# Performance work log

Measured on AMD Instinct MI355X. Metric: run time of the kernel, lower is better.

Reference implementation:

```python
import jax, jax.numpy as jnp
import numpy as np

D_MODEL = 1024
NUM_HEADS = 16
HEAD_DIM = D_MODEL // NUM_HEADS
B, T_Q, T_KV = 4, 4096, 4096


def setup_inputs() -> dict:
    key = jax.random.key(0)
    ks = jax.random.split(key, 10)
    s_in = 1.0 / np.sqrt(D_MODEL)
    s_out = 1.0 / np.sqrt(D_MODEL)
    return {
        "q": jax.random.normal(ks[0], (B, T_Q, D_MODEL), jnp.float32),
        "kv": jax.random.normal(ks[1], (B, T_KV, D_MODEL), jnp.float32),
        # per-head projection weights stacked: [H, d_model, head_dim]
        "Wq": jax.random.uniform(ks[2], (NUM_HEADS, D_MODEL, HEAD_DIM), jnp.float32, -s_in, s_in),
        "bq": jax.random.uniform(ks[3], (NUM_HEADS, HEAD_DIM), jnp.float32, -s_in, s_in),
        "Wk": jax.random.uniform(ks[4], (NUM_HEADS, D_MODEL, HEAD_DIM), jnp.float32, -s_in, s_in),
        "bk": jax.random.uniform(ks[5], (NUM_HEADS, HEAD_DIM), jnp.float32, -s_in, s_in),
        "Wv": jax.random.uniform(ks[6], (NUM_HEADS, D_MODEL, HEAD_DIM), jnp.float32, -s_in, s_in),
        "bv": jax.random.uniform(ks[7], (NUM_HEADS, HEAD_DIM), jnp.float32, -s_in, s_in),
        "Wo": jax.random.uniform(ks[8], (D_MODEL, D_MODEL), jnp.float32, -s_out, s_out),
        "bo": jax.random.uniform(ks[9], (D_MODEL,), jnp.float32, -s_out, s_out),
    }


def reference(q, kv, Wq, bq, Wk, bk, Wv, bv, Wo, bo):
    Bsz, Tq, _ = q.shape
    # per-head projections fused into one batched GEMM each: [b,t,d] x [h,d,e] -> [b,h,t,e]
    qh = jnp.einsum('btd,hde->bhte', q, Wq) + bq[None, :, None, :]
    kh = jnp.einsum('btd,hde->bhte', kv, Wk) + bk[None, :, None, :]
    vh = jnp.einsum('btd,hde->bhte', kv, Wv) + bv[None, :, None, :]
    # squared feature map
    qh = qh * qh
    kh = kh * kh
    # O(N) linear attention aggregation
    kv_sum = jnp.einsum('bhnd,bhne->bhde', kh, vh)           # [B,H,e,e]
    z = 1.0 / (jnp.einsum('bhnd,bhd->bhn', qh, kh.sum(axis=2)) + 1e-6)  # [B,H,Tq]
    attn = jnp.einsum('bhnd,bhde,bhn->bhne', qh, kv_sum, z)  # [B,H,Tq,e]
    attn = attn.transpose(0, 2, 1, 3).reshape(Bsz, Tq, D_MODEL)
    return attn @ Wo.T + bo
```

## Files before the change

kernel.cpp:

```cpp
#include <hip/hip_runtime.h>

#define BSZ 4
#define TSEQ 4096
#define DM 1024
#define NH 16
#define HD 64
#define BT (BSZ * TSEQ)
#define INV_LOSCALE (1.0f / 4096.0f)

using f32x4 = __attribute__((ext_vector_type(4))) float;
using f16x8 = __attribute__((ext_vector_type(8))) _Float16;
using u32x2 = __attribute__((ext_vector_type(2))) unsigned;
using u32x4 = __attribute__((ext_vector_type(4))) unsigned;

typedef const __attribute__((address_space(1))) void* gas_ptr;
typedef __attribute__((address_space(3))) void* las_ptr;

__device__ __forceinline__ void gload16(const void* g, void* l) {
    __builtin_amdgcn_global_load_lds((gas_ptr)g, (las_ptr)l, 16, 0, 0);
}

__device__ __forceinline__ void split1(float x, _Float16& h, _Float16& l) {
    h = (_Float16)x;
    l = (_Float16)((x - (float)h) * 4096.0f);
}
__device__ __forceinline__ unsigned pack2(_Float16 a, _Float16 b) {
    return (unsigned)__builtin_bit_cast(unsigned short, a) |
           ((unsigned)__builtin_bit_cast(unsigned short, b) << 16);
}
__device__ __forceinline__ f32x4 mfma_f16(f16x8 a, f16x8 b, f32x4 c) {
    return __builtin_amdgcn_mfma_f32_16x16x32_f16(a, b, c, 0, 0, 0);
}

__global__ __launch_bounds__(256) void fragsplit_kernel(const float* __restrict__ in,
        _Float16* __restrict__ hi, _Float16* __restrict__ lo) {
    const int C = blockIdx.x * 256 + threadIdx.x;
    const int l15 = C & 15, quad = (C >> 4) & 3, rb = (C >> 6) & 3;
    const int s = (C >> 8) & 31, panel = C >> 13;
    const size_t src = ((size_t)(panel * 64 + rb * 16 + l15)) * DM + s * 32 + quad * 8;
    f32x4 v0 = *(const f32x4*)&in[src];
    f32x4 v1 = *(const f32x4*)&in[src + 4];
    _Float16 h[8], l[8];
    #pragma unroll
    for (int j = 0; j < 4; ++j) { split1(v0[j], h[j], l[j]); split1(v1[j], h[4 + j], l[4 + j]); }
    ((u32x4*)hi)[C] = (u32x4){pack2(h[0],h[1]), pack2(h[2],h[3]), pack2(h[4],h[5]), pack2(h[6],h[7])};
    ((u32x4*)lo)[C] = (u32x4){pack2(l[0],l[1]), pack2(l[2],l[3]), pack2(l[4],l[5]), pack2(l[6],l[7])};
}

__global__ __launch_bounds__(256) void wsplit_kernel(
    const float* __restrict__ Wq, const float* __restrict__ Wk, const float* __restrict__ Wv,
    _Float16* __restrict__ qh, _Float16* __restrict__ ql,
    _Float16* __restrict__ kh, _Float16* __restrict__ kl,
    _Float16* __restrict__ vh, _Float16* __restrict__ vl) {
    const int tid = threadIdx.x;
    const int k0 = blockIdx.x * 64, h = blockIdx.y, w = blockIdx.z;
    const float* __restrict__ W = (w == 0) ? Wq : (w == 1) ? Wk : Wv;
    _Float16* __restrict__ dh = (w == 0) ? qh : (w == 1) ? kh : vh;
    _Float16* __restrict__ dl = (w == 0) ? ql : (w == 1) ? kl : vl;
    __shared__ __align__(16) float ws_[64][68];
    #pragma unroll
    for (int it = 0; it < 4; ++it) {
        int idx = it * 256 + tid;
        int r = idx >> 4, c4 = (idx & 15) * 4;
        *(f32x4*)&ws_[r][c4] = *(const f32x4*)&W[((size_t)h * DM + k0 + r) * HD + c4];
    }
    __syncthreads();
    const int n = tid >> 2, kq16 = (tid & 3) * 16;
    _Float16 hh[16], ll[16];
    #pragma unroll
    for (int j = 0; j < 16; ++j) split1(ws_[kq16 + j][n], hh[j], ll[j]);
    #pragma unroll
    for (int c = 0; c < 2; ++c) {
        int kg = k0 + kq16 + c * 8;
        int s = kg >> 5, quad = (kg >> 3) & 3;
        size_t chunk = (size_t)(h * 32 + s) * 256 + ((n >> 4) * 4 + quad) * 16 + (n & 15);
        ((u32x4*)dh)[chunk] = (u32x4){pack2(hh[c*8+0],hh[c*8+1]), pack2(hh[c*8+2],hh[c*8+3]),
                                      pack2(hh[c*8+4],hh[c*8+5]), pack2(hh[c*8+6],hh[c*8+7])};
        ((u32x4*)dl)[chunk] = (u32x4){pack2(ll[c*8+0],ll[c*8+1]), pack2(ll[c*8+2],ll[c*8+3]),
                                      pack2(ll[c*8+4],ll[c*8+5]), pack2(ll[c*8+6],ll[c*8+7])};
    }
}

__global__ __launch_bounds__(256, 3) void kv_stats_kernel(
    const _Float16* __restrict__ kv_hi, const _Float16* __restrict__ kv_lo,
    const _Float16* __restrict__ wkt_hi, const _Float16* __restrict__ wkt_lo,
    const _Float16* __restrict__ wvt_hi, const _Float16* __restrict__ wvt_lo,
    const float* __restrict__ bk, const float* __restrict__ bv,
    float* __restrict__ kv_sum, float* __restrict__ ksum)
{
    const int tid = threadIdx.x;
    const int lane = tid & 63, wave = tid >> 6, quad = lane >> 4, l15 = lane & 15;
    const int b = blockIdx.z, h = blockIdx.y, bx = blockIdx.x;

    __shared__ __align__(16) char smem[49152];
    float* khs = (float*)smem;
    float* vhs = (float*)(smem + 16384);

    const int isV = wave >> 1, w1 = wave & 1;
    const size_t btile = (size_t)h * 32;
    const int ty = tid >> 4, tx = tid & 15;

    f32x4 akv[4] = {};
    float aks[4] = {0.f, 0.f, 0.f, 0.f};

    for (int sub = 0; sub < 4; ++sub) {
        const size_t atile = (size_t)(b * 64 + bx * 4 + sub) * 32;
        auto stage = [&](int p, int s) {
            char* dst = smem + p * 24576 + tid * 16;
            const size_t ao = (atile + s) * 2048 + tid * 8;
            const size_t bo = (btile + s) * 2048 + tid * 8;
            gload16(&kv_hi[ao],  dst);
            gload16(&kv_lo[ao],  dst + 4096);
            gload16(&wkt_hi[bo], dst + 8192);
            gload16(&wkt_lo[bo], dst + 12288);
            gload16(&wvt_hi[bo], dst + 16384);
            gload16(&wvt_lo[bo], dst + 20480);
        };

        f32x4 acc_h[2][4] = {}, acc_c[2][4] = {};
        stage(0, 0);
        for (int s = 0; s < 32; ++s) {
            const int p = s & 1;
            if (s < 31) {
                stage(p ^ 1, s + 1);
                asm volatile("s_waitcnt vmcnt(6)" ::: "memory");
            } else {
                asm volatile("s_waitcnt vmcnt(0)" ::: "memory");
            }
            __builtin_amdgcn_s_barrier();
            __builtin_amdgcn_sched_barrier(0);
            const char* bufc = smem + p * 24576;
            const _Float16* a_hi = (const _Float16*)bufc;
            const _Float16* a_lo = (const _Float16*)(bufc + 4096);
            const _Float16* bh = (const _Float16*)(bufc + (isV ? 16384 : 8192));
            const _Float16* bl = (const _Float16*)(bufc + (isV ? 20480 : 12288));
            f16x8 afh[2], afl[2], bfh[4], bfl[4];
            #pragma unroll
            for (int mt = 0; mt < 2; ++mt) {
                afh[mt] = *(const f16x8*)&a_hi[(w1 * 2 + mt) * 512 + lane * 8];
                afl[mt] = *(const f16x8*)&a_lo[(w1 * 2 + mt) * 512 + lane * 8];
            }
            #pragma unroll
            for (int nt = 0; nt < 4; ++nt) {
                bfh[nt] = *(const f16x8*)&bh[nt * 512 + lane * 8];
                bfl[nt] = *(const f16x8*)&bl[nt * 512 + lane * 8];
            }
            #pragma unroll
            for (int mt = 0; mt < 2; ++mt)
                #pragma unroll
                for (int nt = 0; nt < 4; ++nt) {
                    acc_h[mt][nt] = mfma_f16(afh[mt], bfh[nt], acc_h[mt][nt]);
                    acc_c[mt][nt] = mfma_f16(afh[mt], bfl[nt], acc_c[mt][nt]);
                    acc_c[mt][nt] = mfma_f16(afl[mt], bfh[nt], acc_c[mt][nt]);
                }
            __builtin_amdgcn_s_barrier();
            __builtin_amdgcn_sched_barrier(0);
        }

        {
            const float* __restrict__ bias = (isV ? bv : bk) + h * HD;
            float* __restrict__ outs = isV ? vhs : khs;
            float bia[4];
            #pragma unroll
            for (int nt = 0; nt < 4; ++nt) bia[nt] = bias[nt * 16 + l15];
            #pragma unroll
            for (int mt = 0; mt < 2; ++mt)
                #pragma unroll
                for (int nt = 0; nt < 4; ++nt)
                    #pragma unroll
                    for (int r = 0; r < 4; ++r) {
                        int t = w1 * 32 + mt * 16 + quad * 4 + r;
                        float v = acc_h[mt][nt][r] + INV_LOSCALE * acc_c[mt][nt][r] + bia[nt];
                        if (!isV) v = v * v;
                        outs[t * 64 + nt * 16 + l15] = v;
                    }
        }
        __syncthreads();

        #pragma unroll 4
        for (int t = 0; t < 64; ++t) {
            f32x4 kd = *(const f32x4*)&khs[t * 64 + ty * 4];
            f32x4 ve = *(const f32x4*)&vhs[t * 64 + tx * 4];
            #pragma unroll
            for (int i = 0; i < 4; ++i) {
                aks[i] += kd[i];
                akv[i] += kd[i] * ve;
            }
        }
        __syncthreads();
    }

    float* kvp = kv_sum + (size_t)(b * NH + h) * HD * HD;
    #pragma unroll
    for (int i = 0; i < 4; ++i)
        #pragma unroll
        for (int j = 0; j < 4; ++j)
            atomicAdd(&kvp[(ty * 4 + i) * HD + tx * 4 + j], akv[i][j]);
    if (tx == 0) {
        float* ksp = ksum + (b * NH + h) * HD;
        #pragma unroll
        for (int i = 0; i < 4; ++i) atomicAdd(&ksp[ty * 4 + i], aks[i]);
    }
}

__global__ __launch_bounds__(256, 3) void q_attn_ps_kernel(
    const _Float16* __restrict__ qf_hi, const _Float16* __restrict__ qf_lo,
    const _Float16* __restrict__ wqt_hi, const _Float16* __restrict__ wqt_lo,
    const float* __restrict__ bq,
    const float* __restrict__ kv_sum, const float* __restrict__ ksum,
    _Float16* __restrict__ attn_hi, _Float16* __restrict__ attn_lo)
{
    const int tid = threadIdx.x;
    const int lane = tid & 63, wave = tid >> 6, quad = lane >> 4, l15 = lane & 15;
    const int b = blockIdx.z, h = blockIdx.y, bx = blockIdx.x;

    __shared__ __align__(16) char smem[32768];
    __shared__ __align__(16) float qs[64 * 68];
    __shared__ float z_s[64], ks_s[64];

    if (tid < 64) ks_s[tid] = ksum[(b * NH + h) * HD + tid];

    const size_t atile = (size_t)(b * 64 + bx) * 32;
    const size_t btile = (size_t)h * 32;

    auto stage = [&](int p, int s) {
        char* dst = smem + p * 16384 + tid * 16;
        const size_t ao = (atile + s) * 2048 + tid * 8;
        const size_t bo = (btile + s) * 2048 + tid * 8;
        gload16(&qf_hi[ao],  dst);
        gload16(&qf_lo[ao],  dst + 4096);
        gload16(&wqt_hi[bo], dst + 8192);
        gload16(&wqt_lo[bo], dst + 12288);
    };

    f32x4 acc_h[4] = {}, acc_c[4] = {};
    stage(0, 0);
    for (int s = 0; s < 32; ++s) {
        const int p = s & 1;
        if (s < 31) {
            stage(p ^ 1, s + 1);
            asm volatile("s_waitcnt vmcnt(4)" ::: "memory");
        } else {
            asm volatile("s_waitcnt vmcnt(0)" ::: "memory");
        }
        __builtin_amdgcn_s_barrier();
        __builtin_amdgcn_sched_barrier(0);
        const char* bufc = smem + p * 16384;
        f16x8 afh = *(const f16x8*)((const _Float16*)bufc + wave * 512 + lane * 8);
        f16x8 afl = *(const f16x8*)((const _Float16*)(bufc + 4096) + wave * 512 + lane * 8);
        f16x8 bfh[4], bfl[4];
        #pragma unroll
        for (int nt = 0; nt < 4; ++nt) {
            bfh[nt] = *(const f16x8*)((const _Float16*)(bufc + 8192) + nt * 512 + lane * 8);
            bfl[nt] = *(const f16x8*)((const _Float16*)(bufc + 12288) + nt * 512 + lane * 8);
        }
        #pragma unroll
        for (int nt = 0; nt < 4; ++nt) {
            acc_h[nt] = mfma_f16(afh, bfh[nt], acc_h[nt]);
            acc_c[nt] = mfma_f16(afh, bfl[nt], acc_c[nt]);
            acc_c[nt] = mfma_f16(afl, bfh[nt], acc_c[nt]);
        }
        __builtin_amdgcn_s_barrier();
        __builtin_amdgcn_sched_barrier(0);
    }

    {
        const int mrow0 = wave * 16;
        const float* __restrict__ bias = bq + h * HD;
        float zp[4] = {0.f, 0.f, 0.f, 0.f};
        #pragma unroll
        for (int nt = 0; nt < 4; ++nt) {
            int d = nt * 16 + l15;
            float bia = bias[d];
            float ks  = ks_s[d];
            #pragma unroll
            for (int r = 0; r < 4; ++r) {
                int t = mrow0 + quad * 4 + r;
                float v = acc_h[nt][r] + INV_LOSCALE * acc_c[nt][r] + bia;
                float v2 = v * v;
                qs[t * 68 + d] = v2;
                zp[r] = fmaf(v2, ks, zp[r]);
            }
        }
        #pragma unroll
        for (int r = 0; r < 4; ++r) {
            float p = zp[r];
            p += __shfl_xor(p, 1);
            p += __shfl_xor(p, 2);
            p += __shfl_xor(p, 4);
            p += __shfl_xor(p, 8);
            if (l15 == 0) z_s[mrow0 + quad * 4 + r] = 1.f / (p + 1e-6f);
        }
    }
    __syncthreads();

    float* kvs = (float*)smem;
    {
        const float* __restrict__ kvp = kv_sum + (size_t)(b * NH + h) * HD * HD;
        #pragma unroll
        for (int it = 0; it < 4; ++it) {
            int idx = it * 256 + tid;
            int r = idx >> 4, c = (idx & 15) * 4;
            *(f32x4*)&kvs[r * 64 + c] = *(const f32x4*)&kvp[r * HD + c];
        }
    }
    __syncthreads();

    const int ty = tid >> 4, tx = tid & 15;
    f32x4 sv[4] = {};
    #pragma unroll 4
    for (int d = 0; d < 64; d += 4) {
        f32x4 b0 = *(const f32x4*)&kvs[(d + 0) * 64 + tx * 4];
        f32x4 b1 = *(const f32x4*)&kvs[(d + 1) * 64 + tx * 4];
        f32x4 b2 = *(const f32x4*)&kvs[(d + 2) * 64 + tx * 4];
        f32x4 b3 = *(const f32x4*)&kvs[(d + 3) * 64 + tx * 4];
        #pragma unroll
        for (int i = 0; i < 4; ++i) {
            f32x4 av = *(const f32x4*)&qs[(ty * 4 + i) * 68 + d];
            sv[i] += av.x * b0 + av.y * b1 + av.z * b2 + av.w * b3;
        }
    }
    const size_t opanel = (size_t)b * 64 + bx;
    const int s_out = h * 2 + (tx >> 3);
    const int kq = (tx >> 1) & 3;
    const int rem8 = (tx & 1) * 8;
    #pragma unroll
    for (int i = 0; i < 4; ++i) {
        int t = ty * 4 + i;
        f32x4 o = sv[i] * z_s[t];
        _Float16 hh[4], ll[4];
        #pragma unroll
        for (int j = 0; j < 4; ++j) split1(o[j], hh[j], ll[j]);
        size_t cb = (((opanel * 32 + s_out) * 256 + ((t >> 4) * 4 + kq) * 16 + (t & 15)) << 4) + rem8;
        *(u32x2*)((char*)attn_hi + cb) = (u32x2){pack2(hh[0], hh[1]), pack2(hh[2], hh[3])};
        *(u32x2*)((char*)attn_lo + cb) = (u32x2){pack2(ll[0], ll[1]), pack2(ll[2], ll[3])};
    }
}

__global__ __launch_bounds__(256, 3) void q_attn_kernel(
    const float* __restrict__ q,
    const _Float16* __restrict__ wqt_hi, const _Float16* __restrict__ wqt_lo,
    const float* __restrict__ bq,
    const float* __restrict__ kv_sum, const float* __restrict__ ksum,
    _Float16* __restrict__ attn_hi, _Float16* __restrict__ attn_lo)
{
    const int tid = threadIdx.x;
    const int lane = tid & 63, wave = tid >> 6, quad = lane >> 4, l15 = lane & 15;
    const int b = blockIdx.z, h = blockIdx.y, bx = blockIdx.x;
    const int t0 = bx * 64;

    __shared__ __align__(16) char smem[32768];
    __shared__ __align__(16) float qs[64 * 68];
    __shared__ float z_s[64], ks_s[64];

    if (tid < 64) ks_s[tid] = ksum[(b * NH + h) * HD + tid];

    const int arb = tid >> 6, aquad = (tid >> 4) & 3, al15 = tid & 15;
    const float* __restrict__ qrow =
        q + ((size_t)b * TSEQ + t0 + arb * 16 + al15) * DM + aquad * 8;
    const size_t btile = (size_t)h * 32;

    auto asplit_write = [&](int p, f32x4 v0, f32x4 v1) {
        _Float16 hh[8], ll[8];
        #pragma unroll
        for (int j = 0; j < 4; ++j) { split1(v0[j], hh[j], ll[j]); split1(v1[j], hh[4+j], ll[4+j]); }
        char* dst = smem + p * 16384 + tid * 16;
        *(u32x4*)dst =
            (u32x4){pack2(hh[0],hh[1]), pack2(hh[2],hh[3]), pack2(hh[4],hh[5]), pack2(hh[6],hh[7])};
        *(u32x4*)(dst + 4096) =
            (u32x4){pack2(ll[0],ll[1]), pack2(ll[2],ll[3]), pack2(ll[4],ll[5]), pack2(ll[6],ll[7])};
    };
    auto stageB = [&](int p, int s) {
        char* dst = smem + p * 16384 + 8192 + tid * 16;
        const size_t bo = (btile + s) * 2048 + tid * 8;
        gload16(&wqt_hi[bo], dst);
        gload16(&wqt_lo[bo], dst + 4096);
    };

    f32x4 acc_h[4] = {}, acc_c[4] = {};
    f32x4 v0 = *(const f32x4*)&qrow[0];
    f32x4 v1 = *(const f32x4*)&qrow[4];
    asplit_write(0, v0, v1);
    stageB(0, 0);
    v0 = *(const f32x4*)&qrow[32];
    v1 = *(const f32x4*)&qrow[36];
    asm volatile("s_waitcnt vmcnt(2) lgkmcnt(0)" ::: "memory");
    __builtin_amdgcn_s_barrier();
    __builtin_amdgcn_sched_barrier(0);

    for (int s = 0; s < 32; ++s) {
        const int p = s & 1;
        if (s < 31) {
            stageB(p ^ 1, s + 1);
            asplit_write(p ^ 1, v0, v1);
            if (s < 30) {
                v0 = *(const f32x4*)&qrow[(s + 2) * 32];
                v1 = *(const f32x4*)&qrow[(s + 2) * 32 + 4];
            }
            asm volatile("s_waitcnt vmcnt(4) lgkmcnt(0)" ::: "memory");
        } else {
            asm volatile("s_waitcnt vmcnt(0)" ::: "memory");
        }
        __builtin_amdgcn_s_barrier();
        __builtin_amdgcn_sched_barrier(0);
        const char* bufc = smem + p * 16384;
        f16x8 afh = *(const f16x8*)((const _Float16*)bufc + wave * 512 + lane * 8);
        f16x8 afl = *(const f16x8*)((const _Float16*)(bufc + 4096) + wave * 512 + lane * 8);
        f16x8 bfh[4], bfl[4];
        #pragma unroll
        for (int nt = 0; nt < 4; ++nt) {
            bfh[nt] = *(const f16x8*)((const _Float16*)(bufc + 8192) + nt * 512 + lane * 8);
            bfl[nt] = *(const f16x8*)((const _Float16*)(bufc + 12288) + nt * 512 + lane * 8);
        }
        #pragma unroll
        for (int nt = 0; nt < 4; ++nt) {
            acc_h[nt] = mfma_f16(afh, bfh[nt], acc_h[nt]);
            acc_c[nt] = mfma_f16(afh, bfl[nt], acc_c[nt]);
            acc_c[nt] = mfma_f16(afl, bfh[nt], acc_c[nt]);
        }
        __builtin_amdgcn_s_barrier();
        __builtin_amdgcn_sched_barrier(0);
    }

    {
        const int mrow0 = wave * 16;
        const float* __restrict__ bias = bq + h * HD;
        float zp[4] = {0.f, 0.f, 0.f, 0.f};
        #pragma unroll
        for (int nt = 0; nt < 4; ++nt) {
            int d = nt * 16 + l15;
            float bia = bias[d];
            float ks  = ks_s[d];
            #pragma unroll
            for (int r = 0; r < 4; ++r) {
                int t = mrow0 + quad * 4 + r;
                float v = acc_h[nt][r] + INV_LOSCALE * acc_c[nt][r] + bia;
                float v2 = v * v;
                qs[t * 68 + d] = v2;
                zp[r] = fmaf(v2, ks, zp[r]);
            }
        }
        #pragma unroll
        for (int r = 0; r < 4; ++r) {
            float p = zp[r];
            p += __shfl_xor(p, 1);
            p += __shfl_xor(p, 2);
            p += __shfl_xor(p, 4);
            p += __shfl_xor(p, 8);
            if (l15 == 0) z_s[mrow0 + quad * 4 + r] = 1.f / (p + 1e-6f);
        }
    }
    __syncthreads();

    float* kvs = (float*)smem;
    {
        const float* __restrict__ kvp = kv_sum + (size_t)(b * NH + h) * HD * HD;
        #pragma unroll
        for (int it = 0; it < 4; ++it) {
            int idx = it * 256 + tid;
            int r = idx >> 4, c = (idx & 15) * 4;
            *(f32x4*)&kvs[r * 64 + c] = *(const f32x4*)&kvp[r * HD + c];
        }
    }
    __syncthreads();

    const int ty = tid >> 4, tx = tid & 15;
    f32x4 sv[4] = {};
    #pragma unroll 4
    for (int d = 0; d < 64; d += 4) {
        f32x4 b0 = *(const f32x4*)&kvs[(d + 0) * 64 + tx * 4];
        f32x4 b1 = *(const f32x4*)&kvs[(d + 1) * 64 + tx * 4];
        f32x4 b2 = *(const f32x4*)&kvs[(d + 2) * 64 + tx * 4];
        f32x4 b3 = *(const f32x4*)&kvs[(d + 3) * 64 + tx * 4];
        #pragma unroll
        for (int i = 0; i < 4; ++i) {
            f32x4 av = *(const f32x4*)&qs[(ty * 4 + i) * 68 + d];
            sv[i] += av.x * b0 + av.y * b1 + av.z * b2 + av.w * b3;
        }
    }
    const size_t opanel = (size_t)b * 64 + bx;
    const int s_out = h * 2 + (tx >> 3);
    const int kq = (tx >> 1) & 3;
    const int rem8 = (tx & 1) * 8;
    #pragma unroll
    for (int i = 0; i < 4; ++i) {
        int t = ty * 4 + i;
        f32x4 o = sv[i] * z_s[t];
        _Float16 hh[4], ll[4];
        #pragma unroll
        for (int j = 0; j < 4; ++j) split1(o[j], hh[j], ll[j]);
        size_t cb = (((opanel * 32 + s_out) * 256 + ((t >> 4) * 4 + kq) * 16 + (t & 15)) << 4) + rem8;
        *(u32x2*)((char*)attn_hi + cb) = (u32x2){pack2(hh[0], hh[1]), pack2(hh[2], hh[3])};
        *(u32x2*)((char*)attn_lo + cb) = (u32x2){pack2(ll[0], ll[1]), pack2(ll[2], ll[3])};
    }
}

__global__ __launch_bounds__(256, 3) void out_proj_kernel(
    const _Float16* __restrict__ attn_hi, const _Float16* __restrict__ attn_lo,
    const _Float16* __restrict__ wo_hi, const _Float16* __restrict__ wo_lo,
    const float* __restrict__ bo, float* __restrict__ out)
{
    const int tid = threadIdx.x;
    const int lane = tid & 63, wave = tid >> 6, quad = lane >> 4, l15 = lane & 15;
    const int n0 = blockIdx.x * 64;
    const size_t m0 = (size_t)blockIdx.y * 128;

    __shared__ __align__(16) char smem[49152];
    float* cs = (float*)smem;

    const size_t ap0 = (m0 >> 6) * 32, ap1 = ap0 + 32;
    const size_t bpn = (size_t)(n0 >> 6) * 32;

    auto stage = [&](int p, int s) {
        char* dst = smem + p * 24576 + tid * 16;
        const size_t co = (size_t)s * 2048 + tid * 8;
        gload16(&attn_hi[ap0 * 2048 + co], dst);
        gload16(&attn_hi[ap1 * 2048 + co], dst + 4096);
        gload16(&attn_lo[ap0 * 2048 + co], dst + 8192);
        gload16(&attn_lo[ap1 * 2048 + co], dst + 12288);
        gload16(&wo_hi[bpn * 2048 + co],  dst + 16384);
        gload16(&wo_lo[bpn * 2048 + co],  dst + 20480);
    };

    const int panel = wave >> 1;
    f32x4 acc_h[2][4] = {}, acc_c[2][4] = {};
    stage(0, 0);
    for (int s = 0; s < 32; ++s) {
        const int p = s & 1;
        if (s < 31) {
            stage(p ^ 1, s + 1);
            asm volatile("s_waitcnt vmcnt(6)" ::: "memory");
        } else {
            asm volatile("s_waitcnt vmcnt(0)" ::: "memory");
        }
        __builtin_amdgcn_s_barrier();
        __builtin_amdgcn_sched_barrier(0);
        const char* bufc = smem + p * 24576;
        f16x8 afh[2], afl[2], bfh[4], bfl[4];
        #pragma unroll
        for (int mt = 0; mt < 2; ++mt) {
            int rbl = (wave & 1) * 2 + mt;
            afh[mt] = *(const f16x8*)((const _Float16*)(bufc + panel * 4096) + rbl * 512 + lane * 8);
            afl[mt] = *(const f16x8*)((const _Float16*)(bufc + 8192 + panel * 4096) + rbl * 512 + lane * 8);
        }
        #pragma unroll
        for (int nt = 0; nt < 4; ++nt) {
            bfh[nt] = *(const f16x8*)((const _Float16*)(bufc + 16384) + nt * 512 + lane * 8);
            bfl[nt] = *(const f16x8*)((const _Float16*)(bufc + 20480) + nt * 512 + lane * 8);
        }
        #pragma unroll
        for (int mt = 0; mt < 2; ++mt)
            #pragma unroll
            for (int nt = 0; nt < 4; ++nt) {
                acc_h[mt][nt] = mfma_f16(afh[mt], bfh[nt], acc_h[mt][nt]);
                acc_c[mt][nt] = mfma_f16(afh[mt], bfl[nt], acc_c[mt][nt]);
                acc_c[mt][nt] = mfma_f16(afl[mt], bfh[nt], acc_c[mt][nt]);
            }
        __builtin_amdgcn_s_barrier();
        __builtin_amdgcn_sched_barrier(0);
    }

    {
        float bia[4];
        #pragma unroll
        for (int nt = 0; nt < 4; ++nt) bia[nt] = bo[n0 + nt * 16 + l15];
        #pragma unroll
        for (int mt = 0; mt < 2; ++mt)
            #pragma unroll
            for (int nt = 0; nt < 4; ++nt)
                #pragma unroll
                for (int r = 0; r < 4; ++r) {
                    int t = wave * 32 + mt * 16 + quad * 4 + r;
                    cs[t * 64 + nt * 16 + l15] =
                        acc_h[mt][nt][r] + INV_LOSCALE * acc_c[mt][nt][r] + bia[nt];
                }
    }
    __syncthreads();
    #pragma unroll
    for (int it = 0; it < 8; ++it) {
        int idx = it * 256 + tid;
        int r = idx >> 4, c = (idx & 15) * 4;
        *(f32x4*)&out[(m0 + r) * DM + n0 + c] = *(f32x4*)&cs[r * 64 + c];
    }
}

extern "C" void kernel_launch(void* const* d_in, const int* in_sizes, int n_in,
                              void* d_out, int out_size, void* d_ws, size_t ws_size,
                              hipStream_t stream) {
    const float* q  = (const float*)d_in[0];
    const float* kv = (const float*)d_in[1];
    const float* Wq = (const float*)d_in[2];
    const float* bq = (const float*)d_in[3];
    const float* Wk = (const float*)d_in[4];
    const float* bk = (const float*)d_in[5];
    const float* Wv = (const float*)d_in[6];
    const float* bv = (const float*)d_in[7];
    const float* Wo = (const float*)d_in[8];
    const float* bo = (const float*)d_in[9];
    float* out = (float*)d_out;

    char* p = (char*)d_ws;
    float* kv_sum = (float*)p;              p += (size_t)BSZ * NH * HD * HD * 4;
    float* ksum   = (float*)p;              p += (size_t)BSZ * NH * HD * 4;
    _Float16* wqt_hi = (_Float16*)p;        p += (size_t)NH * HD * DM * 2;
    _Float16* wqt_lo = (_Float16*)p;        p += (size_t)NH * HD * DM * 2;
    _Float16* wkt_hi = (_Float16*)p;        p += (size_t)NH * HD * DM * 2;
    _Float16* wkt_lo = (_Float16*)p;        p += (size_t)NH * HD * DM * 2;
    _Float16* wvt_hi = (_Float16*)p;        p += (size_t)NH * HD * DM * 2;
    _Float16* wvt_lo = (_Float16*)p;        p += (size_t)NH * HD * DM * 2;
    _Float16* wo_hi  = (_Float16*)p;        p += (size_t)DM * DM * 2;
    _Float16* wo_lo  = (_Float16*)p;        p += (size_t)DM * DM * 2;
    _Float16* buf_hi = (_Float16*)p;        p += (size_t)BT * DM * 2;
    _Float16* buf_lo = (_Float16*)p;        p += (size_t)BT * DM * 2;
    _Float16* qf_hi  = (_Float16*)p;        p += (size_t)BT * DM * 2;
    _Float16* qf_lo  = (_Float16*)p;        p += (size_t)BT * DM * 2;
    const bool big = ws_size >= (size_t)(p - (char*)d_ws);

    size_t zero_bytes = ((size_t)BSZ * NH * HD * HD + (size_t)BSZ * NH * HD) * sizeof(float);
    hipMemsetAsync(d_ws, 0, zero_bytes, stream);

    fragsplit_kernel<<<(BT * DM / 8) / 256, 256, 0, stream>>>(kv, buf_hi, buf_lo);
    wsplit_kernel<<<dim3(DM / 64, NH, 3), 256, 0, stream>>>(
        Wq, Wk, Wv, wqt_hi, wqt_lo, wkt_hi, wkt_lo, wvt_hi, wvt_lo);
    fragsplit_kernel<<<(DM * DM / 8) / 256, 256, 0, stream>>>(Wo, wo_hi, wo_lo);
    if (big)
        fragsplit_kernel<<<(BT * DM / 8) / 256, 256, 0, stream>>>(q, qf_hi, qf_lo);

    kv_stats_kernel<<<dim3(TSEQ / 256, NH, BSZ), 256, 0, stream>>>(
        buf_hi, buf_lo, wkt_hi, wkt_lo, wvt_hi, wvt_lo, bk, bv, kv_sum, ksum);
    if (big)
        q_attn_ps_kernel<<<dim3(TSEQ / 64, NH, BSZ), 256, 0, stream>>>(
            qf_hi, qf_lo, wqt_hi, wqt_lo, bq, kv_sum, ksum, buf_hi, buf_lo);
    else
        q_attn_kernel<<<dim3(TSEQ / 64, NH, BSZ), 256, 0, stream>>>(
            q, wqt_hi, wqt_lo, bq, kv_sum, ksum, buf_hi, buf_lo);
    out_proj_kernel<<<dim3(DM / 64, BT / 128), 256, 0, stream>>>(
        buf_hi, buf_lo, wo_hi, wo_lo, bo, out);
}
```

Before: 735.7 us.

## Double row tiles in kv_stats and q_attn_ps kernels to reuse weight fragments

Both projection GEMM kernels now load two 64-row activation panels per stage, so each staged weight tile is used against twice as many rows. kv_stats processes 128 rows per sub-iteration with 4x4 accumulators per wave and lowers occupancy to 2 blocks; q_attn_ps handles 128 rows per block with half the grid. The aim is to cut redundant weight-tile loads and barrier overhead per row. The cost is higher register and LDS pressure, lower occupancy, and fewer blocks for the q kernel. The q fragsplit launch is also moved after kv_stats.

```diff
diff --git a/kernel.cpp b/kernel.cpp
--- a/kernel.cpp
+++ b/kernel.cpp
@@ -81,7 +81,7 @@
     }
 }
 
-__global__ __launch_bounds__(256, 3) void kv_stats_kernel(
+__global__ __launch_bounds__(256, 2) void kv_stats_kernel(
     const _Float16* __restrict__ kv_hi, const _Float16* __restrict__ kv_lo,
     const _Float16* __restrict__ wkt_hi, const _Float16* __restrict__ wkt_lo,
     const _Float16* __restrict__ wvt_hi, const _Float16* __restrict__ wvt_lo,
@@ -92,53 +92,56 @@
     const int lane = tid & 63, wave = tid >> 6, quad = lane >> 4, l15 = lane & 15;
     const int b = blockIdx.z, h = blockIdx.y, bx = blockIdx.x;
 
-    __shared__ __align__(16) char smem[49152];
+    __shared__ __align__(16) char smem[65536];
     float* khs = (float*)smem;
-    float* vhs = (float*)(smem + 16384);
-
-    const int isV = wave >> 1, w1 = wave & 1;
+    float* vhs = (float*)(smem + 32768);
+
+    const int isV = wave >> 1, half = wave & 1;
     const size_t btile = (size_t)h * 32;
     const int ty = tid >> 4, tx = tid & 15;
 
     f32x4 akv[4] = {};
     float aks[4] = {0.f, 0.f, 0.f, 0.f};
 
-    for (int sub = 0; sub < 4; ++sub) {
-        const size_t atile = (size_t)(b * 64 + bx * 4 + sub) * 32;
+    for (int sub = 0; sub < 2; ++sub) {
+        const size_t apan = (size_t)(b * 64 + bx * 4 + sub * 2);
         auto stage = [&](int p, int s) {
-            char* dst = smem + p * 24576 + tid * 16;
-            const size_t ao = (atile + s) * 2048 + tid * 8;
+            char* dst = smem + p * 32768 + tid * 16;
+            const size_t a0 = (apan * 32 + s) * 2048 + tid * 8;
+            const size_t a1 = ((apan + 1) * 32 + s) * 2048 + tid * 8;
             const size_t bo = (btile + s) * 2048 + tid * 8;
-            gload16(&kv_hi[ao],  dst);
-            gload16(&kv_lo[ao],  dst + 4096);
-            gload16(&wkt_hi[bo], dst + 8192);
-            gload16(&wkt_lo[bo], dst + 12288);
-            gload16(&wvt_hi[bo], dst + 16384);
-            gload16(&wvt_lo[bo], dst + 20480);
+            gload16(&kv_hi[a0], dst);
+            gload16(&kv_hi[a1], dst + 4096);
+            gload16(&kv_lo[a0], dst + 8192);
+            gload16(&kv_lo[a1], dst + 12288);
+            gload16(&wkt_hi[bo], dst + 16384);
+            gload16(&wkt_lo[bo], dst + 20480);
+            gload16(&wvt_hi[bo], dst + 24576);
+            gload16(&wvt_lo[bo], dst + 28672);
         };
 
-        f32x4 acc_h[2][4] = {}, acc_c[2][4] = {};
+        f32x4 acc_h[4][4] = {}, acc_c[4][4] = {};
         stage(0, 0);
         for (int s = 0; s < 32; ++s) {
             const int p = s & 1;
             if (s < 31) {
                 stage(p ^ 1, s + 1);
-                asm volatile("s_waitcnt vmcnt(6)" ::: "memory");
+                asm volatile("s_waitcnt vmcnt(8)" ::: "memory");
             } else {
                 asm volatile("s_waitcnt vmcnt(0)" ::: "memory");
             }
             __builtin_amdgcn_s_barrier();
             __builtin_amdgcn_sched_barrier(0);
-            const char* bufc = smem + p * 24576;
+            const char* bufc = smem + p * 32768;
             const _Float16* a_hi = (const _Float16*)bufc;
-            const _Float16* a_lo = (const _Float16*)(bufc + 4096);
-            const _Float16* bh = (const _Float16*)(bufc + (isV ? 16384 : 8192));
-            const _Float16* bl = (const _Float16*)(bufc + (isV ? 20480 : 12288));
-            f16x8 afh[2], afl[2], bfh[4], bfl[4];
-            #pragma unroll
-            for (int mt = 0; mt < 2; ++mt) {
-                afh[mt] = *(const f16x8*)&a_hi[(w1 * 2 + mt) * 512 + lane * 8];
-                afl[mt] = *(const f16x8*)&a_lo[(w1 * 2 + mt) * 512 + lane * 8];
+            const _Float16* a_lo = (const _Float16*)(bufc + 8192);
+            const _Float16* bh = (const _Float16*)(bufc + (isV ? 24576 : 16384));
+            const _Float16* bl = (const _Float16*)(bufc + (isV ? 28672 : 20480));
+            f16x8 afh[4], afl[4], bfh[4], bfl[4];
+            #pragma unroll
+            for (int mt = 0; mt < 4; ++mt) {
+                afh[mt] = *(const f16x8*)&a_hi[half * 2048 + mt * 512 + lane * 8];
+                afl[mt] = *(const f16x8*)&a_lo[half * 2048 + mt * 512 + lane * 8];
             }
             #pragma unroll
             for (int nt = 0; nt < 4; ++nt) {
@@ -146,7 +149,7 @@
                 bfl[nt] = *(const f16x8*)&bl[nt * 512 + lane * 8];
             }
             #pragma unroll
-            for (int mt = 0; mt < 2; ++mt)
+            for (int mt = 0; mt < 4; ++mt)
                 #pragma unroll
                 for (int nt = 0; nt < 4; ++nt) {
                     acc_h[mt][nt] = mfma_f16(afh[mt], bfh[nt], acc_h[mt][nt]);
@@ -164,12 +167,12 @@
             #pragma unroll
             for (int nt = 0; nt < 4; ++nt) bia[nt] = bias[nt * 16 + l15];
             #pragma unroll
-            for (int mt = 0; mt < 2; ++mt)
+            for (int mt = 0; mt < 4; ++mt)
                 #pragma unroll
                 for (int nt = 0; nt < 4; ++nt)
                     #pragma unroll
                     for (int r = 0; r < 4; ++r) {
-                        int t = w1 * 32 + mt * 16 + quad * 4 + r;
+                        int t = half * 64 + mt * 16 + quad * 4 + r;
                         float v = acc_h[mt][nt][r] + INV_LOSCALE * acc_c[mt][nt][r] + bia[nt];
                         if (!isV) v = v * v;
                         outs[t * 64 + nt * 16 + l15] = v;
@@ -178,7 +181,7 @@
         __syncthreads();
 
         #pragma unroll 4
-        for (int t = 0; t < 64; ++t) {
+        for (int t = 0; t < 128; ++t) {
             f32x4 kd = *(const f32x4*)&khs[t * 64 + ty * 4];
             f32x4 ve = *(const f32x4*)&vhs[t * 64 + tx * 4];
             #pragma unroll
@@ -214,87 +217,101 @@
     const int lane = tid & 63, wave = tid >> 6, quad = lane >> 4, l15 = lane & 15;
     const int b = blockIdx.z, h = blockIdx.y, bx = blockIdx.x;
 
-    __shared__ __align__(16) char smem[32768];
-    __shared__ __align__(16) float qs[64 * 68];
-    __shared__ float z_s[64], ks_s[64];
+    __shared__ __align__(16) char smem[51200];
+    __shared__ float z_s[128], ks_s[64];
 
     if (tid < 64) ks_s[tid] = ksum[(b * NH + h) * HD + tid];
 
-    const size_t atile = (size_t)(b * 64 + bx) * 32;
+    const size_t apan = (size_t)(b * 64 + bx * 2);
     const size_t btile = (size_t)h * 32;
 
     auto stage = [&](int p, int s) {
-        char* dst = smem + p * 16384 + tid * 16;
-        const size_t ao = (atile + s) * 2048 + tid * 8;
+        char* dst = smem + p * 24576 + tid * 16;
+        const size_t a0 = (apan * 32 + s) * 2048 + tid * 8;
+        const size_t a1 = ((apan + 1) * 32 + s) * 2048 + tid * 8;
         const size_t bo = (btile + s) * 2048 + tid * 8;
-        gload16(&qf_hi[ao],  dst);
-        gload16(&qf_lo[ao],  dst + 4096);
-        gload16(&wqt_hi[bo], dst + 8192);
-        gload16(&wqt_lo[bo], dst + 12288);
+        gload16(&qf_hi[a0], dst);
+        gload16(&qf_hi[a1], dst + 4096);
+        gload16(&qf_lo[a0], dst + 8192);
+        gload16(&qf_lo[a1], dst + 12288);
+        gload16(&wqt_hi[bo], dst + 16384);
+        gload16(&wqt_lo[bo], dst + 20480);
     };
 
-    f32x4 acc_h[4] = {}, acc_c[4] = {};
+    f32x4 acc_h[2][4] = {}, acc_c[2][4] = {};
     stage(0, 0);
     for (int s = 0; s < 32; ++s) {
         const int p = s & 1;
         if (s < 31) {
             stage(p ^ 1, s + 1);
-            asm volatile("s_waitcnt vmcnt(4)" ::: "memory");
+            asm volatile("s_waitcnt vmcnt(6)" ::: "memory");
         } else {
             asm volatile("s_waitcnt vmcnt(0)" ::: "memory");
         }
         __builtin_amdgcn_s_barrier();
         __builtin_amdgcn_sched_barrier(0);
-        const char* bufc = smem + p * 16384;
-        f16x8 afh = *(const f16x8*)((const _Float16*)bufc + wave * 512 + lane * 8);
-        f16x8 afl = *(const f16x8*)((const _Float16*)(bufc + 4096) + wave * 512 + lane * 8);
-        f16x8 bfh[4], bfl[4];
+        const char* bufc = smem + p * 24576;
+        const _Float16* a_hi = (const _Float16*)bufc;
+        const _Float16* a_lo = (const _Float16*)(bufc + 8192);
+        f16x8 afh[2], afl[2], bfh[4], bfl[4];
+        #pragma unroll
+        for (int mt = 0; mt < 2; ++mt) {
+            int fo = (wave * 2 + mt) * 512 + lane * 8;
+            afh[mt] = *(const f16x8*)&a_hi[fo];
+            afl[mt] = *(const f16x8*)&a_lo[fo];
+        }
         #pragma unroll
         for (int nt = 0; nt < 4; ++nt) {
-            bfh[nt] = *(const f16x8*)((const _Float16*)(bufc + 8192) + nt * 512 + lane * 8);
-            bfl[nt] = *(const f16x8*)((const _Float16*)(bufc + 12288) + nt * 512 + lane * 8);
-        }
-        #pragma unroll
-        for (int nt = 0; nt < 4; ++nt) {
-            acc_h[nt] = mfma_f16(afh, bfh[nt], acc_h[nt]);
-            acc_c[nt] = mfma_f16(afh, bfl[nt], acc_c[nt]);
-            acc_c[nt] = mfma_f16(afl, bfh[nt], acc_c[nt]);
-        }
+            bfh[nt] = *(const f16x8*)((const _Float16*)(bufc + 16384) + nt * 512 + lane * 8);
+            bfl[nt] = *(const f16x8*)((const _Float16*)(bufc + 20480) + nt * 512 + lane * 8);
+        }
+        #pragma unroll
+        for (int mt = 0; mt < 2; ++mt)
+            #pragma unroll
+            for (int nt = 0; nt < 4; ++nt) {
+                acc_h[mt][nt] = mfma_f16(afh[mt], bfh[nt], acc_h[mt][nt]);
+                acc_c[mt][nt] = mfma_f16(afh[mt], bfl[nt], acc_c[mt][nt]);
+                acc_c[mt][nt] = mfma_f16(afl[mt], bfh[nt], acc_c[mt][nt]);
+            }
         __builtin_amdgcn_s_barrier();
         __builtin_amdgcn_sched_barrier(0);
     }
 
+    float* qs = (float*)smem;
     {
-        const int mrow0 = wave * 16;
         const float* __restrict__ bias = bq + h * HD;
-        float zp[4] = {0.f, 0.f, 0.f, 0.f};
+        float zp[2][4] = {};
         #pragma unroll
         for (int nt = 0; nt < 4; ++nt) {
             int d = nt * 16 + l15;
             float bia = bias[d];
             float ks  = ks_s[d];
             #pragma unroll
+            for (int mt = 0; mt < 2; ++mt)
+                #pragma unroll
+                for (int r = 0; r < 4; ++r) {
+                    int t = wave * 32 + mt * 16 + quad * 4 + r;
+                    float v = acc_h[mt][nt][r] + INV_LOSCALE * acc_c[mt][nt][r] + bia;
+                    float v2 = v * v;
+                    qs[t * 68 + d] = v2;
+                    zp[mt][r] = fmaf(v2, ks, zp[mt][r]);
+                }
+        }
+        #pragma unroll
+        for (int mt = 0; mt < 2; ++mt)
+            #pragma unroll
             for (int r = 0; r < 4; ++r) {
-                int t = mrow0 + quad * 4 + r;
-                float v = acc_h[nt][r] + INV_LOSCALE * acc_c[nt][r] + bia;
-                float v2 = v * v;
-                qs[t * 68 + d] = v2;
-                zp[r] = fmaf(v2, ks, zp[r]);
-            }
-        }
-        #pragma unroll
-        for (int r = 0; r < 4; ++r) {
-            float p = zp[r];
-            p += __shfl_xor(p, 1);
-            p += __shfl_xor(p, 2);
-            p += __shfl_xor(p, 4);
-            p += __shfl_xor(p, 8);
-            if (l15 == 0) z_s[mrow0 + quad * 4 + r] = 1.f / (p + 1e-6f);
-        }
+                float p = zp[mt][r];
+                p += __shfl_xor(p, 1);
+                p += __shfl_xor(p, 2);
+                p += __shfl_xor(p, 4);
+                p += __shfl_xor(p, 8);
+                if (l15 == 0) z_s[wave * 32 + mt * 16 + quad * 4 + r] = 1.f / (p + 1e-6f);
+            }
     }
     __syncthreads();
 
-    float* kvs = (float*)smem;
+    float* kvs = (float*)(smem + 34816);
     {
         const float* __restrict__ kvp = kv_sum + (size_t)(b * NH + h) * HD * HD;
         #pragma unroll
@@ -307,7 +324,7 @@
     __syncthreads();
 
     const int ty = tid >> 4, tx = tid & 15;
-    f32x4 sv[4] = {};
+    f32x4 sv[8] = {};
     #pragma unroll 4
     for (int d = 0; d < 64; d += 4) {
         f32x4 b0 = *(const f32x4*)&kvs[(d + 0) * 64 + tx * 4];
@@ -315,23 +332,24 @@
         f32x4 b2 = *(const f32x4*)&kvs[(d + 2) * 64 + tx * 4];
         f32x4 b3 = *(const f32x4*)&kvs[(d + 3) * 64 + tx * 4];
         #pragma unroll
-        for (int i = 0; i < 4; ++i) {
-            f32x4 av = *(const f32x4*)&qs[(ty * 4 + i) * 68 + d];
+        for (int i = 0; i < 8; ++i) {
+            f32x4 av = *(const f32x4*)&qs[(ty * 8 + i) * 68 + d];
             sv[i] += av.x * b0 + av.y * b1 + av.z * b2 + av.w * b3;
         }
     }
-    const size_t opanel = (size_t)b * 64 + bx;
     const int s_out = h * 2 + (tx >> 3);
     const int kq = (tx >> 1) & 3;
     const int rem8 = (tx & 1) * 8;
     #pragma unroll
-    for (int i = 0; i < 4; ++i) {
-        int t = ty * 4 + i;
+    for (int i = 0; i < 8; ++i) {
+        int t = ty * 8 + i;
+        const size_t opanel = (size_t)b * 64 + bx * 2 + (t >> 6);
+        const int tt = t & 63;
         f32x4 o = sv[i] * z_s[t];
         _Float16 hh[4], ll[4];
         #pragma unroll
         for (int j = 0; j < 4; ++j) split1(o[j], hh[j], ll[j]);
-        size_t cb = (((opanel * 32 + s_out) * 256 + ((t >> 4) * 4 + kq) * 16 + (t & 15)) << 4) + rem8;
+        size_t cb = (((opanel * 32 + s_out) * 256 + ((tt >> 4) * 4 + kq) * 16 + (tt & 15)) << 4) + rem8;
         *(u32x2*)((char*)attn_hi + cb) = (u32x2){pack2(hh[0], hh[1]), pack2(hh[2], hh[3])};
         *(u32x2*)((char*)attn_lo + cb) = (u32x2){pack2(ll[0], ll[1]), pack2(ll[2], ll[3])};
     }
@@ -623,17 +641,18 @@
     wsplit_kernel<<<dim3(DM / 64, NH, 3), 256, 0, stream>>>(
         Wq, Wk, Wv, wqt_hi, wqt_lo, wkt_hi, wkt_lo, wvt_hi, wvt_lo);
     fragsplit_kernel<<<(DM * DM / 8) / 256, 256, 0, stream>>>(Wo, wo_hi, wo_lo);
-    if (big)
-        fragsplit_kernel<<<(BT * DM / 8) / 256, 256, 0, stream>>>(q, qf_hi, qf_lo);
 
     kv_stats_kernel<<<dim3(TSEQ / 256, NH, BSZ), 256, 0, stream>>>(
         buf_hi, buf_lo, wkt_hi, wkt_lo, wvt_hi, wvt_lo, bk, bv, kv_sum, ksum);
-    if (big)
-        q_attn_ps_kernel<<<dim3(TSEQ / 64, NH, BSZ), 256, 0, stream>>>(
+
+    if (big) {
+        fragsplit_kernel<<<(BT * DM / 8) / 256, 256, 0, stream>>>(q, qf_hi, qf_lo);
+        q_attn_ps_kernel<<<dim3(TSEQ / 128, NH, BSZ), 256, 0, stream>>>(
             qf_hi, qf_lo, wqt_hi, wqt_lo, bq, kv_sum, ksum, buf_hi, buf_lo);
-    else
+    } else {
         q_attn_kernel<<<dim3(TSEQ / 64, NH, BSZ), 256, 0, stream>>>(
             q, wqt_hi, wqt_lo, bq, kv_sum, ksum, buf_hi, buf_lo);
+    }
     out_proj_kernel<<<dim3(DM / 64, BT / 128), 256, 0, stream>>>(
         buf_hi, buf_lo, wo_hi, wo_lo, bo, out);
 }
```

Result: faster. 650.5 us (-11.6%).
